# Kernel optimization log

Measured on AMD Instinct MI355X. Metric: run time of the kernel, lower is better.

Reference implementation:

```python
import jax, jax.numpy as jnp
import numpy as np

B, W, D, R = 2, 1024, 1024, 16
GAMMA_FLOOR = 0.85


def setup_inputs() -> dict:
    key = jax.random.key(0)
    ks = jax.random.split(key, 8)
    h = jax.random.normal(ks[0], (B, W, D), jnp.float32)
    # faithful parameter initialization (as in __init__)
    gammas = jnp.linspace(0.95, 0.995, R)
    decay_logit = jnp.log(gammas / (1.0 - gammas))
    pos = jnp.arange(W, dtype=jnp.float32)
    causal = jnp.tril(jnp.ones((W, W), jnp.float32))
    dist0 = jnp.clip(pos[None, :] - pos[:, None], 0.0)  # (j - i)+ , used for k_base init
    k_init = jnp.exp(-0.15 * dist0) * causal
    k_base = k_init / jnp.clip(k_init.sum(axis=1, keepdims=True), 1e-8)
    u = jax.random.normal(ks[1], (D, R), jnp.float32) * 0.05
    v = jax.random.normal(ks[2], (D, R), jnp.float32) * 0.05
    proj_w = jax.random.normal(ks[3], (D, D), jnp.float32) * 0.02
    proj_b = jnp.zeros((D,), jnp.float32)
    up_w = jax.random.normal(ks[4], (D, 2 * D), jnp.float32) * 0.02
    up_b = jnp.zeros((2 * D,), jnp.float32)
    down_w = jax.random.normal(ks[5], (2 * D, D), jnp.float32) * 0.02
    down_b = jnp.zeros((D,), jnp.float32)
    return {
        'h': h,
        'decay_logit': decay_logit,
        'k_base': k_base,
        'k_base_gate_logit': jnp.asarray(8.0, jnp.float32),
        'u': u,
        'v': v,
        'alpha_logit': jnp.asarray(0.0, jnp.float32),
        'proj_w': proj_w,
        'proj_b': proj_b,
        'norm1_scale': jnp.ones((D,), jnp.float32),
        'norm2_scale': jnp.ones((D,), jnp.float32),
        'up_w': up_w,
        'up_b': up_b,
        'down_w': down_w,
        'down_b': down_b,
    }


def _rmsnorm(x, scale, eps=1e-8):
    return x / jnp.sqrt(jnp.mean(x * x, axis=-1, keepdims=True) + eps) * scale


def _l2norm(x, eps=1e-8):
    # matches F.normalize: x / max(||x||, eps)
    n = jnp.sqrt(jnp.sum(x * x, axis=-1, keepdims=True))
    return x / jnp.maximum(n, eps)


def reference(h, decay_logit, k_base, k_base_gate_logit, u, v, alpha_logit,
              proj_w, proj_b, norm1_scale, norm2_scale, up_w, up_b, down_w, down_b):
    b, w, d = h.shape
    pos = jnp.arange(w, dtype=h.dtype)
    causal = jnp.tril(jnp.ones((w, w), h.dtype))

    residual = h
    h_norm = _rmsnorm(h, norm1_scale)

    gate = jax.nn.sigmoid(k_base_gate_logit)
    kb = k_base[:w, :w] * causal * gate
    out = jnp.einsum('ij,bjd->bid', kb, h_norm)

    q = _l2norm(h_norm @ u)  # (b, w, r)
    k = _l2norm(h_norm @ v)  # (b, w, r)

    gamma = GAMMA_FLOOR + (1.0 - GAMMA_FLOOR) * jax.nn.sigmoid(decay_logit)  # (r,)
    alpha = jax.nn.sigmoid(alpha_logit)  # alpha_cap = 1.0

    # decay mask: exp((i-j)+ * log(gamma_r)) on causal entries -> (w, w, r)
    dist = jnp.clip(pos[:, None] - pos[None, :], 0.0)
    log_gamma = jnp.log(jnp.clip(gamma, 1e-8))
    decay_mask = jnp.exp(dist[:, :, None] * log_gamma[None, None, :]) * causal[:, :, None]

    kh = k[..., None] * h_norm[:, :, None, :]  # (b, w, r, d)
    causal_inner = jnp.einsum('ijr,bjrd->bird', decay_mask, kh)  # (b, w, r, d)
    out = out + alpha * jnp.einsum('bwr,bwrd->bwd', q, causal_inner)

    out = out @ proj_w + proj_b
    h2 = residual + out
    h2n = _rmsnorm(h2, norm2_scale)
    mlp = jax.nn.gelu(h2n @ up_w + up_b, approximate=False) @ down_w + down_b
    return h2 + mlp
```

## Files before the change

### kernel.cpp

```cpp
#include <hip/hip_runtime.h>

#define Bv 2
#define Wv 1024
#define Dv 1024
#define Rv 16

typedef __bf16 bf16;
typedef __attribute__((ext_vector_type(8))) __bf16 bf16x8;
typedef __attribute__((ext_vector_type(4))) __bf16 bf16x4;
typedef __attribute__((ext_vector_type(4))) float f32x4;

static __device__ __forceinline__ float sigmoidf_(float x) {
    return 1.0f / (1.0f + expf(-x));
}

static __device__ __forceinline__ void gload_lds16(const void* g, void* l) {
    __builtin_amdgcn_global_load_lds(
        (const __attribute__((address_space(1))) unsigned int*)g,
        (__attribute__((address_space(3))) unsigned int*)l, 16, 0, 0);
}

template <bool INBF16>
__global__ void rmsnorm_kernel(const void* __restrict__ x,
                               const float* __restrict__ scale,
                               bf16* __restrict__ outb) {
    int row = blockIdx.x;
    int t = threadIdx.x;
    float xv[4];
    if (INBF16) {
        bf16x4 v = *(const bf16x4*)((const bf16*)x + (size_t)row * Dv + t * 4);
        xv[0] = (float)v[0]; xv[1] = (float)v[1]; xv[2] = (float)v[2]; xv[3] = (float)v[3];
    } else {
        float4 v = *(const float4*)((const float*)x + (size_t)row * Dv + t * 4);
        xv[0] = v.x; xv[1] = v.y; xv[2] = v.z; xv[3] = v.w;
    }
    float ss = xv[0] * xv[0] + xv[1] * xv[1] + xv[2] * xv[2] + xv[3] * xv[3];
    for (int off = 32; off > 0; off >>= 1) ss += __shfl_down(ss, off);
    __shared__ float wsum[4];
    __shared__ float inv_s;
    int lane = t & 63, wid = t >> 6;
    if (lane == 0) wsum[wid] = ss;
    __syncthreads();
    if (t == 0) {
        float tot = wsum[0] + wsum[1] + wsum[2] + wsum[3];
        inv_s = rsqrtf(tot * (1.0f / Dv) + 1e-8f);
    }
    __syncthreads();
    float inv = inv_s;
    float4 sc = *(const float4*)(scale + t * 4);
    bf16x4 ob = {(bf16)(xv[0] * inv * sc.x), (bf16)(xv[1] * inv * sc.y),
                 (bf16)(xv[2] * inv * sc.z), (bf16)(xv[3] * inv * sc.w)};
    *(bf16x4*)(outb + (size_t)row * Dv + t * 4) = ob;
}

__global__ void prep_kernel(const float* __restrict__ proj_w, const float* __restrict__ up_w,
                            const float* __restrict__ down_w,
                            const float* __restrict__ u, const float* __restrict__ v,
                            const bf16* __restrict__ hnb,
                            bf16* __restrict__ proj_wT, bf16* __restrict__ up_wT,
                            bf16* __restrict__ down_wT, bf16* __restrict__ h_normT,
                            bf16* __restrict__ uvT) {
    __shared__ float tile[32][33];
    int blk = blockIdx.x;
    int t = threadIdx.x;
    if (blk >= 7168) {
        int i = (blk - 7168) * 256 + t;
        int rcol = i >> 10, d = i & (Wv - 1);
        float val = (rcol < Rv) ? u[(size_t)d * Rv + rcol] : v[(size_t)d * Rv + (rcol - Rv)];
        uvT[i] = (bf16)val;
        return;
    }
    const void* src;
    bf16* dst;
    int rows, cols, r0, c0;
    bool f32src = true;
    if (blk < 1024) {
        src = proj_w; dst = proj_wT; rows = 1024; cols = 1024;
        c0 = (blk & 31) * 32; r0 = (blk >> 5) * 32;
    } else if (blk < 3072) {
        int idx = blk - 1024;
        src = up_w; dst = up_wT; rows = 1024; cols = 2048;
        c0 = (idx & 63) * 32; r0 = (idx >> 6) * 32;
    } else if (blk < 5120) {
        int idx = blk - 3072;
        src = down_w; dst = down_wT; rows = 2048; cols = 1024;
        c0 = (idx & 31) * 32; r0 = (idx >> 5) * 32;
    } else {
        int idx = blk - 5120;
        int b = idx >> 10; idx &= 1023;
        src = hnb + (size_t)b * Wv * Dv; dst = h_normT + (size_t)b * Dv * Wv;
        rows = 1024; cols = 1024; f32src = false;
        c0 = (idx & 31) * 32; r0 = (idx >> 5) * 32;
    }
    int r = t >> 3, c4 = (t & 7) * 4;
    float vv[4];
    if (f32src) {
        float4 x = *(const float4*)((const float*)src + (size_t)(r0 + r) * cols + c0 + c4);
        vv[0] = x.x; vv[1] = x.y; vv[2] = x.z; vv[3] = x.w;
    } else {
        bf16x4 x = *(const bf16x4*)((const bf16*)src + (size_t)(r0 + r) * cols + c0 + c4);
        vv[0] = (float)x[0]; vv[1] = (float)x[1]; vv[2] = (float)x[2]; vv[3] = (float)x[3];
    }
    tile[r][c4 + 0] = vv[0];
    tile[r][c4 + 1] = vv[1];
    tile[r][c4 + 2] = vv[2];
    tile[r][c4 + 3] = vv[3];
    __syncthreads();
    int n = t >> 3, k4 = (t & 7) * 4;
    bf16x4 ob = {(bf16)tile[k4 + 0][n], (bf16)tile[k4 + 1][n],
                 (bf16)tile[k4 + 2][n], (bf16)tile[k4 + 3][n]};
    *(bf16x4*)(dst + (size_t)(c0 + n) * rows + r0 + k4) = ob;
}

__global__ __launch_bounds__(256) void qk_mfma(
    const bf16* __restrict__ hnb,
    const bf16* __restrict__ uvT,
    const float* __restrict__ decay_logit,
    bf16* __restrict__ Qs, bf16* __restrict__ Ks) {
    int t = threadIdx.x, lane = t & 63, wid = t >> 6;
    int wm = wid >> 1, wn = wid & 1;
    int row0 = blockIdx.x * 32 + wm * 16;
    const bf16* Arow = hnb + (size_t)(row0 + (lane & 15)) * Dv + (lane >> 4) * 8;
    const bf16* Brow = uvT + (size_t)(wn * 16 + (lane & 15)) * Dv + (lane >> 4) * 8;
    f32x4 acc = {};
#pragma unroll 8
    for (int k0 = 0; k0 < Dv; k0 += 32) {
        bf16x8 a = *(const bf16x8*)(Arow + k0);
        bf16x8 b = *(const bf16x8*)(Brow + k0);
        acc = __builtin_amdgcn_mfma_f32_16x16x32_bf16(a, b, acc, 0, 0, 0);
    }
    int col = lane & 15;
    float dl = decay_logit[col];
    float gamma = 0.85f + 0.15f * sigmoidf_(dl);
    float logg = log2f(gamma);
#pragma unroll
    for (int r = 0; r < 4; ++r) {
        float vv = acc[r];
        float ss = vv * vv;
#pragma unroll
        for (int m = 1; m < 16; m <<= 1) ss += __shfl_xor(ss, m);
        float nrm = fmaxf(sqrtf(ss), 1e-8f);
        float val = vv / nrm;
        int grow = row0 + (lane >> 4) * 4 + r;
        int i = grow & (Wv - 1);
        if (wn == 0) {
            float pw = exp2f((float)i * logg);
            Qs[(size_t)grow * Rv + col] = (bf16)(val * pw);
        } else {
            float pwi = exp2f(-(float)i * logg);
            Ks[(size_t)grow * Rv + col] = (bf16)(val * pwi);
        }
    }
}

__global__ __launch_bounds__(256) void sbuild_mfma(
    const bf16* __restrict__ Qs, const bf16* __restrict__ Ks,
    const float* __restrict__ kbase,
    const float* __restrict__ gate_logit,
    const float* __restrict__ alpha_logit,
    bf16* __restrict__ S) {
    int it = blockIdx.y, jt = blockIdx.x;
    if (jt > it) return;
    int b = blockIdx.z;
    int t = threadIdx.x, lane = t & 63, wid = t >> 6;
    int wm = wid >> 1, wn = wid & 1;
    int i0 = it * 64, j0 = jt * 64;
    int l15 = lane & 15, chunk = lane >> 4;
    bf16x8 af[2], bfr[2];
    bf16x8 z8 = {};
#pragma unroll
    for (int mi = 0; mi < 2; ++mi)
        af[mi] = (chunk < 2)
            ? *(const bf16x8*)(Qs + (size_t)(b * Wv + i0 + wm * 32 + mi * 16 + l15) * Rv + chunk * 8)
            : z8;
#pragma unroll
    for (int ni = 0; ni < 2; ++ni)
        bfr[ni] = (chunk < 2)
            ? *(const bf16x8*)(Ks + (size_t)(b * Wv + j0 + wn * 32 + ni * 16 + l15) * Rv + chunk * 8)
            : z8;
    f32x4 acc[2][2] = {};
#pragma unroll
    for (int mi = 0; mi < 2; ++mi)
#pragma unroll
        for (int ni = 0; ni < 2; ++ni)
            acc[mi][ni] = __builtin_amdgcn_mfma_f32_16x16x32_bf16(af[mi], bfr[ni], acc[mi][ni], 0, 0, 0);
    float gate = sigmoidf_(gate_logit[0]);
    float alpha = sigmoidf_(alpha_logit[0]);
#pragma unroll
    for (int mi = 0; mi < 2; ++mi)
#pragma unroll
        for (int ni = 0; ni < 2; ++ni) {
            int j = j0 + wn * 32 + ni * 16 + l15;
#pragma unroll
            for (int r = 0; r < 4; ++r) {
                int i = i0 + wm * 32 + mi * 16 + chunk * 4 + r;
                float s = (j <= i) ? gate * kbase[(size_t)i * Wv + j] + alpha * acc[mi][ni][r] : 0.f;
                S[((size_t)b * Wv + i) * Wv + j] = (bf16)s;
            }
        }
}

template <bool GELU, bool OUT_BF16, int RES, bool CAUSAL>
__global__ __launch_bounds__(256, 3) void mfma_gemm(
    const bf16* __restrict__ A, const bf16* __restrict__ Bt,
    const float* __restrict__ bias, const void* __restrict__ res,
    void* __restrict__ Cout, int M, int N, int K,
    long sA, long sB, long sC) {
    constexpr int BM = 64, BN = 64, BK = 128;
    __shared__ bf16 As[BM * BK];
    __shared__ bf16 Bs[BN * BK];
    int bz = blockIdx.z;
    A += (size_t)bz * sA;
    Bt += (size_t)bz * sB;
    const int m0 = blockIdx.y * BM, n0 = blockIdx.x * BN;
    const int t = threadIdx.x;
    const int lane = t & 63, wid = t >> 6;
    const int wm = wid >> 1, wn = wid & 1;
    f32x4 acc[2][2] = {};

    const int Klim = CAUSAL ? (m0 + BM < K ? m0 + BM : K) : K;

    const int srow = t >> 4;
    const int fcs = (t & 15) ^ (srow & 7);

    const int q = lane >> 4, s = lane & 7, l15 = lane & 15;

    for (int k0 = 0; k0 < Klim; k0 += BK) {
        __syncthreads();
#pragma unroll
        for (int it = 0; it < 4; ++it) {
            int r = srow + it * 16;
            gload_lds16(A + (size_t)(m0 + r) * K + k0 + fcs * 8,
                        As + it * 2048 + wid * 512);
        }
#pragma unroll
        for (int it = 0; it < 4; ++it) {
            int r = srow + it * 16;
            gload_lds16(Bt + (size_t)(n0 + r) * K + k0 + fcs * 8,
                        Bs + it * 2048 + wid * 512);
        }
        __syncthreads();

        bf16x8 af[2][4], bfr[2][4];
#pragma unroll
        for (int mi = 0; mi < 2; ++mi)
#pragma unroll
            for (int kk = 0; kk < 4; ++kk) {
                af[mi][kk] = *(const bf16x8*)&As[(wm * 32 + mi * 16 + l15) * BK + (((kk * 4 + q) ^ s) * 8)];
                bfr[mi][kk] = *(const bf16x8*)&Bs[(wn * 32 + mi * 16 + l15) * BK + (((kk * 4 + q) ^ s) * 8)];
            }
#pragma unroll
        for (int kk = 0; kk < 4; ++kk)
#pragma unroll
            for (int mi = 0; mi < 2; ++mi)
#pragma unroll
                for (int ni = 0; ni < 2; ++ni)
                    acc[mi][ni] = __builtin_amdgcn_mfma_f32_16x16x32_bf16(
                        af[mi][kk], bfr[ni][kk], acc[mi][ni], 0, 0, 0);
    }

    const int row_base = m0 + wm * 32;
    const int col_base = n0 + wn * 32;
#pragma unroll
    for (int mi = 0; mi < 2; ++mi) {
#pragma unroll
        for (int ni = 0; ni < 2; ++ni) {
            int col = col_base + ni * 16 + l15;
            float bv = bias ? bias[col] : 0.f;
#pragma unroll
            for (int r = 0; r < 4; ++r) {
                int row = row_base + mi * 16 + q * 4 + r;
                float val = acc[mi][ni][r] + bv;
                if (GELU) val = 0.5f * val * (1.0f + erff(val * 0.7071067811865476f));
                if (RES == 1)
                    val += ((const float*)res)[(size_t)bz * sC + (size_t)row * N + col];
                else if (RES == 2)
                    val += (float)((const bf16*)res)[(size_t)bz * sC + (size_t)row * N + col];
                if (OUT_BF16)
                    ((bf16*)Cout)[(size_t)bz * sC + (size_t)row * N + col] = (bf16)val;
                else
                    ((float*)Cout)[(size_t)bz * sC + (size_t)row * N + col] = val;
            }
        }
    }
}

extern "C" void kernel_launch(void* const* d_in, const int* in_sizes, int n_in,
                              void* d_out, int out_size, void* d_ws, size_t ws_size,
                              hipStream_t stream) {
    const float* h = (const float*)d_in[0];
    const float* decay_logit = (const float*)d_in[1];
    const float* k_base = (const float*)d_in[2];
    const float* gate_logit = (const float*)d_in[3];
    const float* u = (const float*)d_in[4];
    const float* v = (const float*)d_in[5];
    const float* alpha_logit = (const float*)d_in[6];
    const float* proj_w = (const float*)d_in[7];
    const float* proj_b = (const float*)d_in[8];
    const float* n1 = (const float*)d_in[9];
    const float* n2 = (const float*)d_in[10];
    const float* up_w = (const float*)d_in[11];
    const float* up_b = (const float*)d_in[12];
    const float* down_w = (const float*)d_in[13];
    const float* down_b = (const float*)d_in[14];
    float* out = (float*)d_out;

    char* ws = (char*)d_ws;
    bf16* hnb = (bf16*)ws;        ws += (size_t)Bv * Wv * Dv * 2;
    bf16* h_normT = (bf16*)ws;    ws += (size_t)Bv * Dv * Wv * 2;
    bf16* uvT = (bf16*)ws;        ws += (size_t)32 * Wv * 2;
    bf16* Qs = (bf16*)ws;         ws += (size_t)Bv * Wv * Rv * 2;
    bf16* Ks = (bf16*)ws;         ws += (size_t)Bv * Wv * Rv * 2;
    bf16* S = (bf16*)ws;          ws += (size_t)Bv * Wv * Wv * 2;
    bf16* out_s = (bf16*)ws;      ws += (size_t)Bv * Wv * Dv * 2;
    bf16* h2b = (bf16*)ws;        ws += (size_t)Bv * Wv * Dv * 2;
    bf16* h2n = (bf16*)ws;        ws += (size_t)Bv * Wv * Dv * 2;
    bf16* g = (bf16*)ws;          ws += (size_t)Bv * Wv * 2 * Dv * 2;
    bf16* proj_wT = (bf16*)ws;    ws += (size_t)Dv * Dv * 2;
    bf16* up_wT = (bf16*)ws;      ws += (size_t)2 * Dv * Dv * 2;
    bf16* down_wT = (bf16*)ws;    ws += (size_t)2 * Dv * Dv * 2;

    int rows = Bv * Wv;

    rmsnorm_kernel<false><<<rows, 256, 0, stream>>>(h, n1, hnb);
    prep_kernel<<<7296, 256, 0, stream>>>(proj_w, up_w, down_w, u, v, hnb,
                                          proj_wT, up_wT, down_wT, h_normT, uvT);
    qk_mfma<<<rows / 32, 256, 0, stream>>>(hnb, uvT, decay_logit, Qs, Ks);
    sbuild_mfma<<<dim3(Wv / 64, Wv / 64, Bv), 256, 0, stream>>>(
        Qs, Ks, k_base, gate_logit, alpha_logit, S);
    mfma_gemm<false, true, 0, true><<<dim3(Dv / 64, Wv / 64, Bv), 256, 0, stream>>>(
        S, h_normT, nullptr, nullptr, out_s, Wv, Dv, Wv,
        (long)Wv * Wv, (long)Dv * Wv, (long)Wv * Dv);
    mfma_gemm<false, true, 1, false><<<dim3(Dv / 64, rows / 64, 1), 256, 0, stream>>>(
        out_s, proj_wT, proj_b, h, h2b, rows, Dv, Dv, 0, 0, 0);
    rmsnorm_kernel<true><<<rows, 256, 0, stream>>>(h2b, n2, h2n);
    mfma_gemm<true, true, 0, false><<<dim3(2 * Dv / 64, rows / 64, 1), 256, 0, stream>>>(
        h2n, up_wT, up_b, nullptr, g, rows, 2 * Dv, Dv, 0, 0, 0);
    mfma_gemm<false, false, 2, false><<<dim3(Dv / 64, rows / 64, 1), 256, 0, stream>>>(
        g, down_wT, down_b, h2b, out, rows, Dv, 2 * Dv, 0, 0, 0);
}
```

Before: 98.06 us.

## Triple-buffer GEMM LDS tiles with async global-to-LDS prefetch pipeline

Replaces the synchronous load-then-compute loop in the MFMA GEMM with a three-stage LDS ring buffer. Loads for future K tiles are issued ahead and waited on with a partial vmcnt, and the K tile shrinks from 128 to 64. The aim is to overlap global memory latency with MFMA work. Dropping the occupancy hint from launch_bounds changes register allocation, and the loop issues redundant clamped loads near the end of K.

```diff
diff --git a/kernel.cpp b/kernel.cpp
--- a/kernel.cpp
+++ b/kernel.cpp
@@ -201,14 +201,14 @@
 }
 
 template <bool GELU, bool OUT_BF16, int RES, bool CAUSAL>
-__global__ __launch_bounds__(256, 3) void mfma_gemm(
+__global__ __launch_bounds__(256) void mfma_gemm(
     const bf16* __restrict__ A, const bf16* __restrict__ Bt,
     const float* __restrict__ bias, const void* __restrict__ res,
     void* __restrict__ Cout, int M, int N, int K,
     long sA, long sB, long sC) {
-    constexpr int BM = 64, BN = 64, BK = 128;
-    __shared__ bf16 As[BM * BK];
-    __shared__ bf16 Bs[BN * BK];
+    constexpr int BM = 64, BN = 64, BK = 64;
+    __shared__ bf16 As[3][BM * BK];
+    __shared__ bf16 Bs[3][BN * BK];
     int bz = blockIdx.z;
     A += (size_t)bz * sA;
     Bt += (size_t)bz * sB;
@@ -219,45 +219,57 @@
     f32x4 acc[2][2] = {};
 
     const int Klim = CAUSAL ? (m0 + BM < K ? m0 + BM : K) : K;
-
-    const int srow = t >> 4;
-    const int fcs = (t & 15) ^ (srow & 7);
+    const int nt = Klim >> 6;
+
+    const int fr0 = t >> 3;
+    const int fcs = (t & 7) ^ (fr0 & 7);
+    const bf16* Asrc = A + (size_t)(m0 + fr0) * K + fcs * 8;
+    const bf16* Bsrc = Bt + (size_t)(n0 + fr0) * K + fcs * 8;
 
     const int q = lane >> 4, s = lane & 7, l15 = lane & 15;
 
-    for (int k0 = 0; k0 < Klim; k0 += BK) {
-        __syncthreads();
-#pragma unroll
-        for (int it = 0; it < 4; ++it) {
-            int r = srow + it * 16;
-            gload_lds16(A + (size_t)(m0 + r) * K + k0 + fcs * 8,
-                        As + it * 2048 + wid * 512);
-        }
-#pragma unroll
-        for (int it = 0; it < 4; ++it) {
-            int r = srow + it * 16;
-            gload_lds16(Bt + (size_t)(n0 + r) * K + k0 + fcs * 8,
-                        Bs + it * 2048 + wid * 512);
-        }
-        __syncthreads();
-
-        bf16x8 af[2][4], bfr[2][4];
+#define STAGE(sb, kt)                                                        \
+    do {                                                                     \
+        const bf16* a_ = Asrc + (size_t)(kt) * BK;                           \
+        const bf16* b_ = Bsrc + (size_t)(kt) * BK;                           \
+        gload_lds16(a_, &As[sb][wid * 512]);                                 \
+        gload_lds16(a_ + (size_t)32 * K, &As[sb][2048 + wid * 512]);         \
+        gload_lds16(b_, &Bs[sb][wid * 512]);                                 \
+        gload_lds16(b_ + (size_t)32 * K, &Bs[sb][2048 + wid * 512]);         \
+    } while (0)
+
+    STAGE(0, 0);
+    STAGE(1, nt > 1 ? 1 : nt - 1);
+    STAGE(2, nt > 2 ? 2 : nt - 1);
+
+    int cur = 0;
+    for (int tt = 0; tt < nt; ++tt) {
+        asm volatile("s_waitcnt vmcnt(8)" ::: "memory");
+        __builtin_amdgcn_s_barrier();
+
+        bf16x8 af[2][2], bfr[2][2];
 #pragma unroll
         for (int mi = 0; mi < 2; ++mi)
 #pragma unroll
-            for (int kk = 0; kk < 4; ++kk) {
-                af[mi][kk] = *(const bf16x8*)&As[(wm * 32 + mi * 16 + l15) * BK + (((kk * 4 + q) ^ s) * 8)];
-                bfr[mi][kk] = *(const bf16x8*)&Bs[(wn * 32 + mi * 16 + l15) * BK + (((kk * 4 + q) ^ s) * 8)];
+            for (int kk = 0; kk < 2; ++kk) {
+                af[mi][kk] = *(const bf16x8*)&As[cur][(wm * 32 + mi * 16 + l15) * BK + (((kk * 4 + q) ^ s) * 8)];
+                bfr[mi][kk] = *(const bf16x8*)&Bs[cur][(wn * 32 + mi * 16 + l15) * BK + (((kk * 4 + q) ^ s) * 8)];
             }
 #pragma unroll
-        for (int kk = 0; kk < 4; ++kk)
+        for (int kk = 0; kk < 2; ++kk)
 #pragma unroll
             for (int mi = 0; mi < 2; ++mi)
 #pragma unroll
                 for (int ni = 0; ni < 2; ++ni)
                     acc[mi][ni] = __builtin_amdgcn_mfma_f32_16x16x32_bf16(
                         af[mi][kk], bfr[ni][kk], acc[mi][ni], 0, 0, 0);
-    }
+
+        __builtin_amdgcn_s_barrier();
+        int kn = (tt + 3 < nt) ? tt + 3 : nt - 1;
+        STAGE(cur, kn);
+        cur = (cur == 2) ? 0 : cur + 1;
+    }
+#undef STAGE
 
     const int row_base = m0 + wm * 32;
     const int col_base = n0 + wn * 32;
```

Measured after the change: 104.7 us. 1.07x slower.

## Fold RMSNorm scales into weights and GEMM epilogues instead of materializing normalized activations

Applied to the files above, without the earlier changes.

Removes both standalone RMSNorm kernels. The norm1/norm2 scale vectors are folded into the transposed weights (u/v and up_w), and the per-row inverse RMS factors are applied in the Q/K, S-build and GEMM epilogues as row or column scales. The first norm's row reductions are merged into the prep kernel, so the raw h is transposed directly and the qk kernel reads fp32 h. This saves one kernel launch and one full bf16 activation write/read per norm. In exchange the qk kernel reads twice the bytes, and rounding changes because unnormalized h is cast to bf16.

```diff
diff --git a/kernel.cpp b/kernel.cpp
--- a/kernel.cpp
+++ b/kernel.cpp
@@ -20,66 +20,49 @@
         (__attribute__((address_space(3))) unsigned int*)l, 16, 0, 0);
 }
 
-template <bool INBF16>
-__global__ void rmsnorm_kernel(const void* __restrict__ x,
-                               const float* __restrict__ scale,
-                               bf16* __restrict__ outb) {
-    int row = blockIdx.x;
-    int t = threadIdx.x;
-    float xv[4];
-    if (INBF16) {
-        bf16x4 v = *(const bf16x4*)((const bf16*)x + (size_t)row * Dv + t * 4);
-        xv[0] = (float)v[0]; xv[1] = (float)v[1]; xv[2] = (float)v[2]; xv[3] = (float)v[3];
-    } else {
-        float4 v = *(const float4*)((const float*)x + (size_t)row * Dv + t * 4);
-        xv[0] = v.x; xv[1] = v.y; xv[2] = v.z; xv[3] = v.w;
-    }
-    float ss = xv[0] * xv[0] + xv[1] * xv[1] + xv[2] * xv[2] + xv[3] * xv[3];
-    for (int off = 32; off > 0; off >>= 1) ss += __shfl_down(ss, off);
-    __shared__ float wsum[4];
-    __shared__ float inv_s;
-    int lane = t & 63, wid = t >> 6;
-    if (lane == 0) wsum[wid] = ss;
-    __syncthreads();
-    if (t == 0) {
-        float tot = wsum[0] + wsum[1] + wsum[2] + wsum[3];
-        inv_s = rsqrtf(tot * (1.0f / Dv) + 1e-8f);
-    }
-    __syncthreads();
-    float inv = inv_s;
-    float4 sc = *(const float4*)(scale + t * 4);
-    bf16x4 ob = {(bf16)(xv[0] * inv * sc.x), (bf16)(xv[1] * inv * sc.y),
-                 (bf16)(xv[2] * inv * sc.z), (bf16)(xv[3] * inv * sc.w)};
-    *(bf16x4*)(outb + (size_t)row * Dv + t * 4) = ob;
-}
-
-__global__ void prep_kernel(const float* __restrict__ proj_w, const float* __restrict__ up_w,
+__global__ void prep_kernel(const float* __restrict__ h,
+                            const float* __restrict__ proj_w, const float* __restrict__ up_w,
                             const float* __restrict__ down_w,
                             const float* __restrict__ u, const float* __restrict__ v,
-                            const bf16* __restrict__ hnb,
+                            const float* __restrict__ n1, const float* __restrict__ n2,
                             bf16* __restrict__ proj_wT, bf16* __restrict__ up_wT,
-                            bf16* __restrict__ down_wT, bf16* __restrict__ h_normT,
-                            bf16* __restrict__ uvT) {
+                            bf16* __restrict__ down_wT, bf16* __restrict__ hT,
+                            bf16* __restrict__ uvT, float* __restrict__ inv1g) {
     __shared__ float tile[32][33];
+    __shared__ float wsum[4];
     int blk = blockIdx.x;
     int t = threadIdx.x;
+    if (blk >= 7296) {
+        int row = blk - 7296;
+        float4 x = *(const float4*)(h + (size_t)row * Dv + t * 4);
+        float ss = x.x * x.x + x.y * x.y + x.z * x.z + x.w * x.w;
+        for (int off = 32; off > 0; off >>= 1) ss += __shfl_down(ss, off);
+        int lane = t & 63, wid = t >> 6;
+        if (lane == 0) wsum[wid] = ss;
+        __syncthreads();
+        if (t == 0) {
+            float tot = wsum[0] + wsum[1] + wsum[2] + wsum[3];
+            inv1g[row] = rsqrtf(tot * (1.0f / Dv) + 1e-8f);
+        }
+        return;
+    }
     if (blk >= 7168) {
         int i = (blk - 7168) * 256 + t;
         int rcol = i >> 10, d = i & (Wv - 1);
         float val = (rcol < Rv) ? u[(size_t)d * Rv + rcol] : v[(size_t)d * Rv + (rcol - Rv)];
-        uvT[i] = (bf16)val;
+        uvT[i] = (bf16)(val * n1[d]);
         return;
     }
-    const void* src;
+    const float* src;
+    const float* rscale = nullptr;
     bf16* dst;
     int rows, cols, r0, c0;
-    bool f32src = true;
     if (blk < 1024) {
         src = proj_w; dst = proj_wT; rows = 1024; cols = 1024;
         c0 = (blk & 31) * 32; r0 = (blk >> 5) * 32;
     } else if (blk < 3072) {
         int idx = blk - 1024;
-        src = up_w; dst = up_wT; rows = 1024; cols = 2048;
+        src = up_w; dst = up_wT; rows = 1024; cols = 2048; rscale = n2;
         c0 = (idx & 63) * 32; r0 = (idx >> 6) * 32;
     } else if (blk < 5120) {
         int idx = blk - 3072;
@@ -88,23 +71,17 @@
     } else {
         int idx = blk - 5120;
         int b = idx >> 10; idx &= 1023;
-        src = hnb + (size_t)b * Wv * Dv; dst = h_normT + (size_t)b * Dv * Wv;
-        rows = 1024; cols = 1024; f32src = false;
+        src = h + (size_t)b * Wv * Dv; dst = hT + (size_t)b * Dv * Wv;
+        rows = 1024; cols = 1024;
         c0 = (idx & 31) * 32; r0 = (idx >> 5) * 32;
     }
     int r = t >> 3, c4 = (t & 7) * 4;
-    float vv[4];
-    if (f32src) {
-        float4 x = *(const float4*)((const float*)src + (size_t)(r0 + r) * cols + c0 + c4);
-        vv[0] = x.x; vv[1] = x.y; vv[2] = x.z; vv[3] = x.w;
-    } else {
-        bf16x4 x = *(const bf16x4*)((const bf16*)src + (size_t)(r0 + r) * cols + c0 + c4);
-        vv[0] = (float)x[0]; vv[1] = (float)x[1]; vv[2] = (float)x[2]; vv[3] = (float)x[3];
-    }
-    tile[r][c4 + 0] = vv[0];
-    tile[r][c4 + 1] = vv[1];
-    tile[r][c4 + 2] = vv[2];
-    tile[r][c4 + 3] = vv[3];
+    float4 x = *(const float4*)(src + (size_t)(r0 + r) * cols + c0 + c4);
+    float sc = rscale ? rscale[r0 + r] : 1.0f;
+    tile[r][c4 + 0] = x.x * sc;
+    tile[r][c4 + 1] = x.y * sc;
+    tile[r][c4 + 2] = x.z * sc;
+    tile[r][c4 + 3] = x.w * sc;
     __syncthreads();
     int n = t >> 3, k4 = (t & 7) * 4;
     bf16x4 ob = {(bf16)tile[k4 + 0][n], (bf16)tile[k4 + 1][n],
@@ -112,20 +89,41 @@
     *(bf16x4*)(dst + (size_t)(c0 + n) * rows + r0 + k4) = ob;
 }
 
+__global__ void inv2_kernel(const bf16* __restrict__ x, float* __restrict__ inv2g) {
+    int row = blockIdx.x;
+    int t = threadIdx.x;
+    bf16x4 vb = *(const bf16x4*)(x + (size_t)row * Dv + t * 4);
+    float a0 = (float)vb[0], a1 = (float)vb[1], a2 = (float)vb[2], a3 = (float)vb[3];
+    float ss = a0 * a0 + a1 * a1 + a2 * a2 + a3 * a3;
+    for (int off = 32; off > 0; off >>= 1) ss += __shfl_down(ss, off);
+    __shared__ float wsum[4];
+    int lane = t & 63, wid = t >> 6;
+    if (lane == 0) wsum[wid] = ss;
+    __syncthreads();
+    if (t == 0) {
+        float tot = wsum[0] + wsum[1] + wsum[2] + wsum[3];
+        inv2g[row] = rsqrtf(tot * (1.0f / Dv) + 1e-8f);
+    }
+}
+
 __global__ __launch_bounds__(256) void qk_mfma(
-    const bf16* __restrict__ hnb,
+    const float* __restrict__ h,
     const bf16* __restrict__ uvT,
     const float* __restrict__ decay_logit,
+    const float* __restrict__ inv1g,
     bf16* __restrict__ Qs, bf16* __restrict__ Ks) {
     int t = threadIdx.x, lane = t & 63, wid = t >> 6;
     int wm = wid >> 1, wn = wid & 1;
     int row0 = blockIdx.x * 32 + wm * 16;
-    const bf16* Arow = hnb + (size_t)(row0 + (lane & 15)) * Dv + (lane >> 4) * 8;
+    const float* Arow = h + (size_t)(row0 + (lane & 15)) * Dv + (lane >> 4) * 8;
     const bf16* Brow = uvT + (size_t)(wn * 16 + (lane & 15)) * Dv + (lane >> 4) * 8;
     f32x4 acc = {};
 #pragma unroll 8
     for (int k0 = 0; k0 < Dv; k0 += 32) {
-        bf16x8 a = *(const bf16x8*)(Arow + k0);
+        float4 a0 = *(const float4*)(Arow + k0);
+        float4 a1 = *(const float4*)(Arow + k0 + 4);
+        bf16x8 a = {(bf16)a0.x, (bf16)a0.y, (bf16)a0.z, (bf16)a0.w,
+                    (bf16)a1.x, (bf16)a1.y, (bf16)a1.z, (bf16)a1.w};
         bf16x8 b = *(const bf16x8*)(Brow + k0);
         acc = __builtin_amdgcn_mfma_f32_16x16x32_bf16(a, b, acc, 0, 0, 0);
     }
@@ -147,7 +145,7 @@
             float pw = exp2f((float)i * logg);
             Qs[(size_t)grow * Rv + col] = (bf16)(val * pw);
         } else {
-            float pwi = exp2f(-(float)i * logg);
+            float pwi = exp2f(-(float)i * logg) * inv1g[grow];
             Ks[(size_t)grow * Rv + col] = (bf16)(val * pwi);
         }
     }
@@ -158,6 +156,7 @@
     const float* __restrict__ kbase,
     const float* __restrict__ gate_logit,
     const float* __restrict__ alpha_logit,
+    const float* __restrict__ inv1g,
     bf16* __restrict__ S) {
     int it = blockIdx.y, jt = blockIdx.x;
     if (jt > it) return;
@@ -191,19 +190,21 @@
 #pragma unroll
         for (int ni = 0; ni < 2; ++ni) {
             int j = j0 + wn * 32 + ni * 16 + l15;
+            float invj = inv1g[b * Wv + j];
 #pragma unroll
             for (int r = 0; r < 4; ++r) {
                 int i = i0 + wm * 32 + mi * 16 + chunk * 4 + r;
-                float s = (j <= i) ? gate * kbase[(size_t)i * Wv + j] + alpha * acc[mi][ni][r] : 0.f;
+                float s = (j <= i) ? gate * kbase[(size_t)i * Wv + j] * invj + alpha * acc[mi][ni][r] : 0.f;
                 S[((size_t)b * Wv + i) * Wv + j] = (bf16)s;
             }
         }
 }
 
-template <bool GELU, bool OUT_BF16, int RES, bool CAUSAL>
+template <bool GELU, bool OUT_BF16, int RES, bool CAUSAL, bool RS, bool CS>
 __global__ __launch_bounds__(256, 3) void mfma_gemm(
     const bf16* __restrict__ A, const bf16* __restrict__ Bt,
     const float* __restrict__ bias, const void* __restrict__ res,
+    const float* __restrict__ rowscale, const float* __restrict__ colscale,
     void* __restrict__ Cout, int M, int N, int K,
     long sA, long sB, long sC) {
     constexpr int BM = 64, BN = 64, BK = 128;
@@ -267,10 +268,14 @@
         for (int ni = 0; ni < 2; ++ni) {
             int col = col_base + ni * 16 + l15;
             float bv = bias ? bias[col] : 0.f;
+            float cs = CS ? colscale[col] : 1.0f;
 #pragma unroll
             for (int r = 0; r < 4; ++r) {
                 int row = row_base + mi * 16 + q * 4 + r;
-                float val = acc[mi][ni][r] + bv;
+                float val = acc[mi][ni][r];
+                if (RS) val *= rowscale[row];
+                if (CS) val *= cs;
+                val += bv;
                 if (GELU) val = 0.5f * val * (1.0f + erff(val * 0.7071067811865476f));
                 if (RES == 1)
                     val += ((const float*)res)[(size_t)bz * sC + (size_t)row * N + col];
@@ -306,15 +311,15 @@
     float* out = (float*)d_out;
 
     char* ws = (char*)d_ws;
-    bf16* hnb = (bf16*)ws;        ws += (size_t)Bv * Wv * Dv * 2;
-    bf16* h_normT = (bf16*)ws;    ws += (size_t)Bv * Dv * Wv * 2;
+    bf16* hT = (bf16*)ws;         ws += (size_t)Bv * Dv * Wv * 2;
     bf16* uvT = (bf16*)ws;        ws += (size_t)32 * Wv * 2;
     bf16* Qs = (bf16*)ws;         ws += (size_t)Bv * Wv * Rv * 2;
     bf16* Ks = (bf16*)ws;         ws += (size_t)Bv * Wv * Rv * 2;
+    float* inv1g = (float*)ws;    ws += (size_t)Bv * Wv * 4;
+    float* inv2g = (float*)ws;    ws += (size_t)Bv * Wv * 4;
     bf16* S = (bf16*)ws;          ws += (size_t)Bv * Wv * Wv * 2;
     bf16* out_s = (bf16*)ws;      ws += (size_t)Bv * Wv * Dv * 2;
     bf16* h2b = (bf16*)ws;        ws += (size_t)Bv * Wv * Dv * 2;
-    bf16* h2n = (bf16*)ws;        ws += (size_t)Bv * Wv * Dv * 2;
     bf16* g = (bf16*)ws;          ws += (size_t)Bv * Wv * 2 * Dv * 2;
     bf16* proj_wT = (bf16*)ws;    ws += (size_t)Dv * Dv * 2;
     bf16* up_wT = (bf16*)ws;      ws += (size_t)2 * Dv * Dv * 2;
@@ -322,20 +327,19 @@
 
     int rows = Bv * Wv;
 
-    rmsnorm_kernel<false><<<rows, 256, 0, stream>>>(h, n1, hnb);
-    prep_kernel<<<7296, 256, 0, stream>>>(proj_w, up_w, down_w, u, v, hnb,
-                                          proj_wT, up_wT, down_wT, h_normT, uvT);
-    qk_mfma<<<rows / 32, 256, 0, stream>>>(hnb, uvT, decay_logit, Qs, Ks);
+    prep_kernel<<<9344, 256, 0, stream>>>(h, proj_w, up_w, down_w, u, v, n1, n2,
+                                          proj_wT, up_wT, down_wT, hT, uvT, inv1g);
+    qk_mfma<<<rows / 32, 256, 0, stream>>>(h, uvT, decay_logit, inv1g, Qs, Ks);
     sbuild_mfma<<<dim3(Wv / 64, Wv / 64, Bv), 256, 0, stream>>>(
-        Qs, Ks, k_base, gate_logit, alpha_logit, S);
-    mfma_gemm<false, true, 0, true><<<dim3(Dv / 64, Wv / 64, Bv), 256, 0, stream>>>(
-        S, h_normT, nullptr, nullptr, out_s, Wv, Dv, Wv,
+        Qs, Ks, k_base, gate_logit, alpha_logit, inv1g, S);
+    mfma_gemm<false, true, 0, true, false, true><<<dim3(Dv / 64, Wv / 64, Bv), 256, 0, stream>>>(
+        S, hT, nullptr, nullptr, nullptr, n1, out_s, Wv, Dv, Wv,
         (long)Wv * Wv, (long)Dv * Wv, (long)Wv * Dv);
-    mfma_gemm<false, true, 1, false><<<dim3(Dv / 64, rows / 64, 1), 256, 0, stream>>>(
-        out_s, proj_wT, proj_b, h, h2b, rows, Dv, Dv, 0, 0, 0);
-    rmsnorm_kernel<true><<<rows, 256, 0, stream>>>(h2b, n2, h2n);
-    mfma_gemm<true, true, 0, false><<<dim3(2 * Dv / 64, rows / 64, 1), 256, 0, stream>>>(
-        h2n, up_wT, up_b, nullptr, g, rows, 2 * Dv, Dv, 0, 0, 0);
-    mfma_gemm<false, false, 2, false><<<dim3(Dv / 64, rows / 64, 1), 256, 0, stream>>>(
-        g, down_wT, down_b, h2b, out, rows, Dv, 2 * Dv, 0, 0, 0);
-}
+    mfma_gemm<false, true, 1, false, false, false><<<dim3(Dv / 64, rows / 64, 1), 256, 0, stream>>>(
+        out_s, proj_wT, proj_b, h, nullptr, nullptr, h2b, rows, Dv, Dv, 0, 0, 0);
+    inv2_kernel<<<rows, 256, 0, stream>>>(h2b, inv2g);
+    mfma_gemm<true, true, 0, false, true, false><<<dim3(2 * Dv / 64, rows / 64, 1), 256, 0, stream>>>(
+        h2b, up_wT, up_b, nullptr, inv2g, nullptr, g, rows, 2 * Dv, Dv, 0, 0, 0);
+    mfma_gemm<false, false, 2, false, false, false><<<dim3(Dv / 64, rows / 64, 1), 256, 0, stream>>>(
+        g, down_wT, down_b, h2b, nullptr, nullptr, out, rows, Dv, 2 * Dv, 0, 0, 0);
+}
```

Result: slower. 105.9 us (+8.0%).

## Fold second RMSNorm into up-proj GEMM and swizzle GEMM block order

Applied to the files above, without the earlier changes.

The second RMSNorm no longer writes a normalized bf16 copy. The norm2 scale is folded into the transposed up_w weights during prep, a small kernel computes only per-row inverse RMS, and the up-proj GEMM multiplies each accumulator by that row scale in its epilogue. This removes one full activation write and read. Separately, every mfma_gemm now remaps its flat block index with an 8-way interleave, aiming for better cache locality across XCDs. Rounding order changes slightly because normalization is now applied after the bf16 GEMM instead of before.

```diff
diff --git a/kernel.cpp b/kernel.cpp
--- a/kernel.cpp
+++ b/kernel.cpp
@@ -20,21 +20,13 @@
         (__attribute__((address_space(3))) unsigned int*)l, 16, 0, 0);
 }
 
-template <bool INBF16>
-__global__ void rmsnorm_kernel(const void* __restrict__ x,
+__global__ void rmsnorm_kernel(const float* __restrict__ x,
                                const float* __restrict__ scale,
                                bf16* __restrict__ outb) {
     int row = blockIdx.x;
     int t = threadIdx.x;
-    float xv[4];
-    if (INBF16) {
-        bf16x4 v = *(const bf16x4*)((const bf16*)x + (size_t)row * Dv + t * 4);
-        xv[0] = (float)v[0]; xv[1] = (float)v[1]; xv[2] = (float)v[2]; xv[3] = (float)v[3];
-    } else {
-        float4 v = *(const float4*)((const float*)x + (size_t)row * Dv + t * 4);
-        xv[0] = v.x; xv[1] = v.y; xv[2] = v.z; xv[3] = v.w;
-    }
-    float ss = xv[0] * xv[0] + xv[1] * xv[1] + xv[2] * xv[2] + xv[3] * xv[3];
+    float4 v = *(const float4*)(x + (size_t)row * Dv + t * 4);
+    float ss = v.x * v.x + v.y * v.y + v.z * v.z + v.w * v.w;
     for (int off = 32; off > 0; off >>= 1) ss += __shfl_down(ss, off);
     __shared__ float wsum[4];
     __shared__ float inv_s;
@@ -48,14 +40,32 @@
     __syncthreads();
     float inv = inv_s;
     float4 sc = *(const float4*)(scale + t * 4);
-    bf16x4 ob = {(bf16)(xv[0] * inv * sc.x), (bf16)(xv[1] * inv * sc.y),
-                 (bf16)(xv[2] * inv * sc.z), (bf16)(xv[3] * inv * sc.w)};
+    bf16x4 ob = {(bf16)(v.x * inv * sc.x), (bf16)(v.y * inv * sc.y),
+                 (bf16)(v.z * inv * sc.z), (bf16)(v.w * inv * sc.w)};
     *(bf16x4*)(outb + (size_t)row * Dv + t * 4) = ob;
+}
+
+__global__ void inv2_kernel(const bf16* __restrict__ x, float* __restrict__ inv2g) {
+    int row = blockIdx.x;
+    int t = threadIdx.x;
+    bf16x4 vb = *(const bf16x4*)(x + (size_t)row * Dv + t * 4);
+    float a0 = (float)vb[0], a1 = (float)vb[1], a2 = (float)vb[2], a3 = (float)vb[3];
+    float ss = a0 * a0 + a1 * a1 + a2 * a2 + a3 * a3;
+    for (int off = 32; off > 0; off >>= 1) ss += __shfl_down(ss, off);
+    __shared__ float wsum[4];
+    int lane = t & 63, wid = t >> 6;
+    if (lane == 0) wsum[wid] = ss;
+    __syncthreads();
+    if (t == 0) {
+        float tot = wsum[0] + wsum[1] + wsum[2] + wsum[3];
+        inv2g[row] = rsqrtf(tot * (1.0f / Dv) + 1e-8f);
+    }
 }
 
 __global__ void prep_kernel(const float* __restrict__ proj_w, const float* __restrict__ up_w,
                             const float* __restrict__ down_w,
                             const float* __restrict__ u, const float* __restrict__ v,
+                            const float* __restrict__ n2,
                             const bf16* __restrict__ hnb,
                             bf16* __restrict__ proj_wT, bf16* __restrict__ up_wT,
                             bf16* __restrict__ down_wT, bf16* __restrict__ h_normT,
@@ -71,6 +81,7 @@
         return;
     }
     const void* src;
+    const float* rscale = nullptr;
     bf16* dst;
     int rows, cols, r0, c0;
     bool f32src = true;
@@ -79,7 +90,7 @@
         c0 = (blk & 31) * 32; r0 = (blk >> 5) * 32;
     } else if (blk < 3072) {
         int idx = blk - 1024;
-        src = up_w; dst = up_wT; rows = 1024; cols = 2048;
+        src = up_w; dst = up_wT; rows = 1024; cols = 2048; rscale = n2;
         c0 = (idx & 63) * 32; r0 = (idx >> 6) * 32;
     } else if (blk < 5120) {
         int idx = blk - 3072;
@@ -101,10 +112,11 @@
         bf16x4 x = *(const bf16x4*)((const bf16*)src + (size_t)(r0 + r) * cols + c0 + c4);
         vv[0] = (float)x[0]; vv[1] = (float)x[1]; vv[2] = (float)x[2]; vv[3] = (float)x[3];
     }
-    tile[r][c4 + 0] = vv[0];
-    tile[r][c4 + 1] = vv[1];
-    tile[r][c4 + 2] = vv[2];
-    tile[r][c4 + 3] = vv[3];
+    float sc = rscale ? rscale[r0 + r] : 1.0f;
+    tile[r][c4 + 0] = vv[0] * sc;
+    tile[r][c4 + 1] = vv[1] * sc;
+    tile[r][c4 + 2] = vv[2] * sc;
+    tile[r][c4 + 3] = vv[3] * sc;
     __syncthreads();
     int n = t >> 3, k4 = (t & 7) * 4;
     bf16x4 ob = {(bf16)tile[k4 + 0][n], (bf16)tile[k4 + 1][n],
@@ -200,19 +212,30 @@
         }
 }
 
-template <bool GELU, bool OUT_BF16, int RES, bool CAUSAL>
+template <bool GELU, bool OUT_BF16, int RES, bool CAUSAL, bool RS>
 __global__ __launch_bounds__(256, 3) void mfma_gemm(
     const bf16* __restrict__ A, const bf16* __restrict__ Bt,
     const float* __restrict__ bias, const void* __restrict__ res,
+    const float* __restrict__ rowscale,
     void* __restrict__ Cout, int M, int N, int K,
     long sA, long sB, long sC) {
     constexpr int BM = 64, BN = 64, BK = 128;
     __shared__ bf16 As[BM * BK];
     __shared__ bf16 Bs[BN * BK];
-    int bz = blockIdx.z;
+
+    const int gx = gridDim.x, gy = gridDim.y;
+    int flat = blockIdx.x + gx * (blockIdx.y + gy * blockIdx.z);
+    const int nwg = gx * gy * gridDim.z;
+    const int cpx = nwg >> 3;
+    int swz = (flat & 7) * cpx + (flat >> 3);
+    const int bx = swz % gx;
+    int tmp = swz / gx;
+    const int by = tmp % gy;
+    const int bz = tmp / gy;
+
     A += (size_t)bz * sA;
     Bt += (size_t)bz * sB;
-    const int m0 = blockIdx.y * BM, n0 = blockIdx.x * BN;
+    const int m0 = by * BM, n0 = bx * BN;
     const int t = threadIdx.x;
     const int lane = t & 63, wid = t >> 6;
     const int wm = wid >> 1, wn = wid & 1;
@@ -270,7 +293,9 @@
 #pragma unroll
             for (int r = 0; r < 4; ++r) {
                 int row = row_base + mi * 16 + q * 4 + r;
-                float val = acc[mi][ni][r] + bv;
+                float val = acc[mi][ni][r];
+                if (RS) val *= rowscale[row];
+                val += bv;
                 if (GELU) val = 0.5f * val * (1.0f + erff(val * 0.7071067811865476f));
                 if (RES == 1)
                     val += ((const float*)res)[(size_t)bz * sC + (size_t)row * N + col];
@@ -311,10 +336,10 @@
     bf16* uvT = (bf16*)ws;        ws += (size_t)32 * Wv * 2;
     bf16* Qs = (bf16*)ws;         ws += (size_t)Bv * Wv * Rv * 2;
     bf16* Ks = (bf16*)ws;         ws += (size_t)Bv * Wv * Rv * 2;
+    float* inv2g = (float*)ws;    ws += (size_t)Bv * Wv * 4;
     bf16* S = (bf16*)ws;          ws += (size_t)Bv * Wv * Wv * 2;
     bf16* out_s = (bf16*)ws;      ws += (size_t)Bv * Wv * Dv * 2;
     bf16* h2b = (bf16*)ws;        ws += (size_t)Bv * Wv * Dv * 2;
-    bf16* h2n = (bf16*)ws;        ws += (size_t)Bv * Wv * Dv * 2;
     bf16* g = (bf16*)ws;          ws += (size_t)Bv * Wv * 2 * Dv * 2;
     bf16* proj_wT = (bf16*)ws;    ws += (size_t)Dv * Dv * 2;
     bf16* up_wT = (bf16*)ws;      ws += (size_t)2 * Dv * Dv * 2;
@@ -322,20 +347,20 @@
 
     int rows = Bv * Wv;
 
-    rmsnorm_kernel<false><<<rows, 256, 0, stream>>>(h, n1, hnb);
-    prep_kernel<<<7296, 256, 0, stream>>>(proj_w, up_w, down_w, u, v, hnb,
+    rmsnorm_kernel<<<rows, 256, 0, stream>>>(h, n1, hnb);
+    prep_kernel<<<7296, 256, 0, stream>>>(proj_w, up_w, down_w, u, v, n2, hnb,
                                           proj_wT, up_wT, down_wT, h_normT, uvT);
     qk_mfma<<<rows / 32, 256, 0, stream>>>(hnb, uvT, decay_logit, Qs, Ks);
     sbuild_mfma<<<dim3(Wv / 64, Wv / 64, Bv), 256, 0, stream>>>(
         Qs, Ks, k_base, gate_logit, alpha_logit, S);
-    mfma_gemm<false, true, 0, true><<<dim3(Dv / 64, Wv / 64, Bv), 256, 0, stream>>>(
-        S, h_normT, nullptr, nullptr, out_s, Wv, Dv, Wv,
+    mfma_gemm<false, true, 0, true, false><<<dim3(Dv / 64, Wv / 64, Bv), 256, 0, stream>>>(
+        S, h_normT, nullptr, nullptr, nullptr, out_s, Wv, Dv, Wv,
         (long)Wv * Wv, (long)Dv * Wv, (long)Wv * Dv);
-    mfma_gemm<false, true, 1, false><<<dim3(Dv / 64, rows / 64, 1), 256, 0, stream>>>(
-        out_s, proj_wT, proj_b, h, h2b, rows, Dv, Dv, 0, 0, 0);
-    rmsnorm_kernel<true><<<rows, 256, 0, stream>>>(h2b, n2, h2n);
-    mfma_gemm<true, true, 0, false><<<dim3(2 * Dv / 64, rows / 64, 1), 256, 0, stream>>>(
-        h2n, up_wT, up_b, nullptr, g, rows, 2 * Dv, Dv, 0, 0, 0);
-    mfma_gemm<false, false, 2, false><<<dim3(Dv / 64, rows / 64, 1), 256, 0, stream>>>(
-        g, down_wT, down_b, h2b, out, rows, Dv, 2 * Dv, 0, 0, 0);
-}
+    mfma_gemm<false, true, 1, false, false><<<dim3(Dv / 64, rows / 64, 1), 256, 0, stream>>>(
+        out_s, proj_wT, proj_b, h, nullptr, h2b, rows, Dv, Dv, 0, 0, 0);
+    inv2_kernel<<<rows, 256, 0, stream>>>(h2b, inv2g);
+    mfma_gemm<true, true, 0, false, true><<<dim3(2 * Dv / 64, rows / 64, 1), 256, 0, stream>>>(
+        h2b, up_wT, up_b, nullptr, inv2g, g, rows, 2 * Dv, Dv, 0, 0, 0);
+    mfma_gemm<false, false, 2, false, false><<<dim3(Dv / 64, rows / 64, 1), 256, 0, stream>>>(
+        g, down_wT, down_b, h2b, nullptr, out, rows, Dv, 2 * Dv, 0, 0, 0);
+}
```

Result: no change. 97.44 us (-0.6%).
